# Kernel optimization log

Hardware: AMD Instinct MI355X
Metric: run time of the kernel (lower is better)

## Reference

```python
import jax, jax.numpy as jnp
import numpy as np

RENORM_PERIOD = 256
MAX_NORM = 100.0


def setup_inputs() -> dict:
    key = jax.random.key(0)
    ks = jax.random.split(key, 9)
    B, S, G, D, N = 4, 2048, 8, 128, 64
    return {
        "x_r": jax.random.normal(ks[0], (B, S, G, D), jnp.float32),
        "x_i": jax.random.normal(ks[1], (B, S, G, D), jnp.float32),
        "log_A_mag": jax.random.uniform(ks[2], (G, N), jnp.float32) * 0.5 + 0.5,
        "A_phase": jax.random.normal(ks[3], (G, N), jnp.float32) * 0.1,
        "Bw_r": jax.random.normal(ks[4], (N, D), jnp.float32) / np.sqrt(D),
        "Bw_i": jax.random.normal(ks[5], (N, D), jnp.float32) / np.sqrt(D),
        "Cw_r": jax.random.normal(ks[6], (D, N), jnp.float32) / np.sqrt(N),
        "Cw_i": jax.random.normal(ks[7], (D, N), jnp.float32) / np.sqrt(N),
        "dt_w": jax.random.normal(ks[8], (2, 2 * D), jnp.float32) * 0.02,
        "dt_b": jnp.zeros((2,), jnp.float32),
    }


def reference(x_r, x_i, log_A_mag, A_phase, Bw_r, Bw_i, Cw_r, Cw_i, dt_w, dt_b):
    B, S, G, D = x_r.shape
    N = Bw_r.shape[0]
    # dt: input-dependent step magnitude / phase scale, clamped
    x_cat = jnp.concatenate([x_r, x_i], axis=-1)            # [B,S,G,2D]
    dt = jnp.clip(jnp.exp(jnp.einsum('bsgd,od->bsgo', x_cat, dt_w) + dt_b), 1e-4, 2.0)
    dt_mag = dt[..., 0:1]                                    # [B,S,G,1]
    dt_phase = dt[..., 1:2]
    # A_bar in polar form, |A| = exp(-softplus(log_A_mag)*dt_mag) < 1
    neg_log_A = -jax.nn.softplus(log_A_mag)[None, None]      # [1,1,G,N]
    A_mag = jnp.exp(dt_mag * neg_log_A)                      # [B,S,G,N]
    A_ang = dt_phase * A_phase[None, None]
    A_r = A_mag * jnp.cos(A_ang)
    A_i = A_mag * jnp.sin(A_ang)
    # Bx = (B_proj @ x) * dt_mag, complex linear
    Bx_r = (jnp.einsum('bsgd,nd->bsgn', x_r, Bw_r) - jnp.einsum('bsgd,nd->bsgn', x_i, Bw_i)) * dt_mag
    Bx_i = (jnp.einsum('bsgd,nd->bsgn', x_r, Bw_i) + jnp.einsum('bsgd,nd->bsgn', x_i, Bw_r)) * dt_mag

    def step(carry, inp):
        h_r, h_i = carry
        ar, ai, br, bi, t = inp
        nh_r = ar * h_r - ai * h_i + br
        nh_i = ar * h_i + ai * h_r + bi
        renorm = ((t + 1) % RENORM_PERIOD) == 0
        norm = jnp.sqrt(nh_r * nh_r + nh_i * nh_i + 1e-8)
        scale = jnp.minimum(norm, MAX_NORM) / norm
        nh_r = jnp.where(renorm, nh_r * scale, nh_r)
        nh_i = jnp.where(renorm, nh_i * scale, nh_i)
        return (nh_r, nh_i), (nh_r, nh_i)

    h0 = (jnp.zeros((B, G, N), jnp.float32), jnp.zeros((B, G, N), jnp.float32))
    xs = (jnp.moveaxis(A_r, 1, 0), jnp.moveaxis(A_i, 1, 0),
          jnp.moveaxis(Bx_r, 1, 0), jnp.moveaxis(Bx_i, 1, 0),
          jnp.arange(S))
    _, (all_h_r, all_h_i) = jax.lax.scan(step, h0, xs)       # [S,B,G,N]
    all_h_r = jnp.moveaxis(all_h_r, 0, 1)                    # [B,S,G,N]
    all_h_i = jnp.moveaxis(all_h_i, 0, 1)
    # y = C_proj(h), complex linear N -> D
    y_r = jnp.einsum('bsgn,dn->bsgd', all_h_r, Cw_r) - jnp.einsum('bsgn,dn->bsgd', all_h_i, Cw_i)
    y_i = jnp.einsum('bsgn,dn->bsgd', all_h_r, Cw_i) + jnp.einsum('bsgn,dn->bsgd', all_h_i, Cw_r)
    return jnp.stack([y_r, y_i], axis=0)                     # [2,B,S,G,D]
```

## Files before the change

### kernel.cpp

```cpp
#include <hip/hip_runtime.h>
#include <math.h>

#define B_ 4
#define S_ 2048
#define G_ 8
#define D_ 128
#define N_ 64
#define ROWS (B_*S_*G_)
#define CH 64
#define CLEN 32
#define NCHAIN (B_*G_*N_)
#define YOFF (ROWS*D_)

typedef short bf16x8 __attribute__((ext_vector_type(8)));
typedef float f32x4  __attribute__((ext_vector_type(4)));
#define MFMA16(a,b,c) __builtin_amdgcn_mfma_f32_16x16x32_bf16(a,b,c,0,0,0)

__device__ __forceinline__ unsigned short bf16_rtne(float f) {
    unsigned u = __float_as_uint(f);
    unsigned r = (u + 0x7FFFu + ((u >> 16) & 1u)) >> 16;
    return (unsigned short)r;
}
__device__ __forceinline__ void split_bf16(float f, unsigned short &hi, unsigned short &lo) {
    hi = bf16_rtne(f);
    float hif = __uint_as_float(((unsigned)hi) << 16);
    lo = bf16_rtne(f - hif);
}
__device__ __forceinline__ unsigned pk_bf16(float a, float b) {
    unsigned r;
    asm("v_cvt_pk_bf16_f32 %0, %1, %2" : "=v"(r) : "v"(a), "v"(b));
    return r;
}
__device__ __forceinline__ void split4_pk(float4 v, uint2 &hi2, uint2 &lo2) {
    unsigned p0 = pk_bf16(v.x, v.y);
    unsigned p1 = pk_bf16(v.z, v.w);
    float r0 = v.x - __uint_as_float(p0 << 16);
    float r1 = v.y - __uint_as_float(p0 & 0xFFFF0000u);
    float r2 = v.z - __uint_as_float(p1 << 16);
    float r3 = v.w - __uint_as_float(p1 & 0xFFFF0000u);
    hi2 = make_uint2(p0, p1);
    lo2 = make_uint2(pk_bf16(r0, r1), pk_bf16(r2, r3));
}
__device__ __forceinline__ float dot4(float4 a, float4 b) {
    return fmaf(a.x,b.x, fmaf(a.y,b.y, fmaf(a.z,b.z, a.w*b.w)));
}

__global__ __launch_bounds__(256) void k_prep(
    const float* __restrict__ bwr, const float* __restrict__ bwi,
    const float* __restrict__ cwr, const float* __restrict__ cwi,
    unsigned short* __restrict__ wbhi, unsigned short* __restrict__ wblo,
    unsigned short* __restrict__ wchi)
{
    int tid = blockIdx.x * 256 + threadIdx.x;
    if (tid < 4096) {
        int f = tid;
        int lane = f & 63, ks = (f >> 6) & 7, nt = (f >> 9) & 1, w = f >> 10;
        int l15 = lane & 15, quad = lane >> 4;
        int n = w * 32 + nt * 16 + l15;
        int k0 = ks * 32 + quad * 8;
        const float* src; float sgn = 1.f;
        if (n < 64) {
            if (k0 < 128) src = bwr + n * 128 + k0;
            else        { src = bwi + n * 128 + (k0 - 128); sgn = -1.f; }
        } else {
            if (k0 < 128) src = bwi + (n - 64) * 128 + k0;
            else          src = bwr + (n - 64) * 128 + (k0 - 128);
        }
        float4 v0 = *(const float4*)src;
        float4 v1 = *(const float4*)(src + 4);
        float vv[8] = {v0.x,v0.y,v0.z,v0.w,v1.x,v1.y,v1.z,v1.w};
        unsigned short h[8], l[8];
        #pragma unroll
        for (int j = 0; j < 8; j++) split_bf16(vv[j] * sgn, h[j], l[j]);
        #pragma unroll
        for (int j = 0; j < 8; j++) { wbhi[f*8+j] = h[j]; wblo[f*8+j] = l[j]; }
    } else {
        int f = tid - 4096;
        int lane = f & 63, ks = (f >> 6) & 3, nt = (f >> 8) & 3, w = f >> 10;
        int l15 = lane & 15, quad = lane >> 4;
        int n = w * 64 + nt * 16 + l15;
        int d = (n < 128) ? n : (n - 128);
        int k0 = ks * 32 + quad * 8;
        unsigned short h[8];
        #pragma unroll
        for (int j = 0; j < 8; j++) {
            int k = k0 + j, col = k >> 1;
            float val;
            if (n < 128) val = (k & 1) ? -cwi[d * 64 + col] : cwr[d * 64 + col];
            else         val = (k & 1) ?  cwr[d * 64 + col] : cwi[d * 64 + col];
            unsigned short hh, hl; split_bf16(val, hh, hl);
            h[j] = hh;
        }
        #pragma unroll
        for (int j = 0; j < 8; j++) wchi[f*8+j] = h[j];
    }
}

#define LDK1 280
__global__ __launch_bounds__(256, 4) void k_g1(
    const float* __restrict__ xr, const float* __restrict__ xi,
    const float* __restrict__ dtw, const float* __restrict__ dtb,
    const float* __restrict__ logAm, const float* __restrict__ Aph,
    const unsigned short* __restrict__ wbhi, const unsigned short* __restrict__ wblo,
    float* __restrict__ bxr, float* __restrict__ bxi,
    float* __restrict__ dt_mag, float* __restrict__ dt_ph,
    float4* __restrict__ trans)
{
    __shared__ __align__(16) unsigned short Ahi[32 * LDK1];
    __shared__ __align__(16) unsigned short Alo[32 * LDK1];
    __shared__ float dms[32], dps[32];
    __shared__ float4 comb[64];
    float* bxs = (float*)Ahi;
    const int t = threadIdx.x;
    const int lane = t & 63, w = t >> 6;
    const int l15 = lane & 15, quad = lane >> 4;
    const int bg = blockIdx.x >> 6, c = blockIdx.x & 63;
    const int g = bg & 7, b = bg >> 3;
    const int crow = (bg * CH + c) * CLEN;

    const int kq = t & 31, k4 = kq * 4;
    float4 w0r = *(const float4*)(dtw + k4);
    float4 w0i = *(const float4*)(dtw + 128 + k4);
    float4 w1r = *(const float4*)(dtw + 256 + k4);
    float4 w1i = *(const float4*)(dtw + 384 + k4);
    float b0 = dtb[0], b1 = dtb[1];
    float nla = -logf(1.0f + __expf(logAm[g * N_ + lane]));
    float aph = Aph[g * N_ + lane];

    const int s0 = c * CLEN;
    const float* xrb = xr + ((size_t)(b * S_ + s0) * G_ + g) * 128;
    const float* xib = xi + ((size_t)(b * S_ + s0) * G_ + g) * 128;

    float pm[4], pp[4];
    #pragma unroll
    for (int i = 0; i < 4; i++) {
        int f = t + 256 * i;
        int m = f >> 5, kk = f & 31;
        float4 a  = ((const float4*)(xrb + m * 1024))[kk];
        float4 bb = ((const float4*)(xib + m * 1024))[kk];
        uint2 h2, l2;
        split4_pk(a, h2, l2);
        *(uint2*)&Ahi[m * LDK1 + kk * 4] = h2;
        *(uint2*)&Alo[m * LDK1 + kk * 4] = l2;
        split4_pk(bb, h2, l2);
        *(uint2*)&Ahi[m * LDK1 + 128 + kk * 4] = h2;
        *(uint2*)&Alo[m * LDK1 + 128 + kk * 4] = l2;
        pm[i] = dot4(a, w0r) + dot4(bb, w0i);
        pp[i] = dot4(a, w1r) + dot4(bb, w1i);
    }
    #pragma unroll
    for (int i = 0; i < 4; i++) {
        float vm = pm[i], vp = pp[i];
        #pragma unroll
        for (int msk = 16; msk >= 1; msk >>= 1) {
            vm += __shfl_xor(vm, msk);
            vp += __shfl_xor(vp, msk);
        }
        if ((t & 31) == 0) {
            int m = (t >> 5) + 8 * i;
            float dm = fminf(fmaxf(__expf(vm + b0), 1e-4f), 2.0f);
            float dp = fminf(fmaxf(__expf(vp + b1), 1e-4f), 2.0f);
            dms[m] = dm; dps[m] = dp;
            dt_mag[crow + m] = dm; dt_ph[crow + m] = dp;
        }
    }
    __syncthreads();

    f32x4 acc[2][2];
    #pragma unroll
    for (int a = 0; a < 2; a++)
        #pragma unroll
        for (int bq = 0; bq < 2; bq++)
            acc[a][bq] = (f32x4){0.f, 0.f, 0.f, 0.f};
    #pragma unroll
    for (int ks = 0; ks < 8; ks++) {
        bf16x8 wh0 = ((const bf16x8*)wbhi)[((w * 2 + 0) * 8 + ks) * 64 + lane];
        bf16x8 wl0 = ((const bf16x8*)wblo)[((w * 2 + 0) * 8 + ks) * 64 + lane];
        bf16x8 wh1 = ((const bf16x8*)wbhi)[((w * 2 + 1) * 8 + ks) * 64 + lane];
        bf16x8 wl1 = ((const bf16x8*)wblo)[((w * 2 + 1) * 8 + ks) * 64 + lane];
        #pragma unroll
        for (int ms = 0; ms < 2; ms++) {
            int arow = (ms * 16 + l15) * LDK1 + quad * 8;
            bf16x8 ah = *(const bf16x8*)&Ahi[arow + ks * 32];
            bf16x8 al = *(const bf16x8*)&Alo[arow + ks * 32];
            acc[ms][0] = MFMA16(al, wh0, acc[ms][0]);
            acc[ms][0] = MFMA16(ah, wl0, acc[ms][0]);
            acc[ms][0] = MFMA16(ah, wh0, acc[ms][0]);
            acc[ms][1] = MFMA16(al, wh1, acc[ms][1]);
            acc[ms][1] = MFMA16(ah, wl1, acc[ms][1]);
            acc[ms][1] = MFMA16(ah, wh1, acc[ms][1]);
        }
    }
    __syncthreads();

    #pragma unroll
    for (int ms = 0; ms < 2; ms++)
        #pragma unroll
        for (int nt = 0; nt < 2; nt++) {
            int n = w * 32 + nt * 16 + l15;
            float* dstg = (n < 64) ? bxr : bxi;
            int nn = n & 63;
            #pragma unroll
            for (int r = 0; r < 4; r++) {
                int m = ms * 16 + quad * 4 + r;
                float v = acc[ms][nt][r] * dms[m];
                dstg[(crow + m) * 64 + nn] = v;
                bxs[m * 132 + n] = v;
            }
        }
    __syncthreads();

    float Ar = 1.f, Ai = 0.f, Br = 0.f, Bi = 0.f;
    if (w < 2) {
        int base = w * 16;
        #pragma unroll
        for (int tt = 0; tt < 16; tt++) {
            int m = base + tt;
            float dm = dms[m], dp = dps[m];
            float am  = __expf(dm * nla);
            float ang = dp * aph;
            float cr = am * __cosf(ang), ci = am * __sinf(ang);
            float vr = bxs[m * 132 + lane], vi = bxs[m * 132 + 64 + lane];
            float nAr = cr * Ar - ci * Ai;
            float nAi = cr * Ai + ci * Ar;
            float nBr = cr * Br - ci * Bi + vr;
            float nBi = cr * Bi + ci * Br + vi;
            Ar = nAr; Ai = nAi; Br = nBr; Bi = nBi;
        }
        if (w == 0) comb[lane] = make_float4(Ar, Ai, Br, Bi);
    }
    __syncthreads();
    if (w == 1) {
        float4 c0 = comb[lane];
        float fAr = Ar * c0.x - Ai * c0.y;
        float fAi = Ar * c0.y + Ai * c0.x;
        float fBr = Ar * c0.z - Ai * c0.w + Br;
        float fBi = Ar * c0.w + Ai * c0.z + Bi;
        trans[(bg * CH + c) * 64 + lane] = make_float4(fAr, fAi, fBr, fBi);
    }
}

__global__ __launch_bounds__(256) void k_scanB2(const float4* __restrict__ trans,
    float2* __restrict__ hstart)
{
    int w = threadIdx.x >> 6, lane = threadIdx.x & 63;
    int W = blockIdx.x * 4 + w;
    int bg = W >> 3;
    int n  = ((W & 7) << 3) + (lane & 7);
    int j  = lane >> 3;
    float pAr[8], pAi[8], pBr[8], pBi[8];
    float Ar = 1.f, Ai = 0.f, Br = 0.f, Bi = 0.f;
    const float4* tp = trans + (bg * CH + j * 8) * 64 + n;
    #pragma unroll
    for (int k = 0; k < 8; k++) {
        pAr[k] = Ar; pAi[k] = Ai; pBr[k] = Br; pBi[k] = Bi;
        float4 T = tp[k * 64];
        float nAr = T.x * Ar - T.y * Ai;
        float nAi = T.x * Ai + T.y * Ar;
        float nBr = T.x * Br - T.y * Bi + T.z;
        float nBi = T.x * Bi + T.y * Br + T.w;
        Ar = nAr; Ai = nAi; Br = nBr; Bi = nBi;
    }
    float hr = 0.f, hi = 0.f, mhr = 0.f, mhi = 0.f;
    #pragma unroll
    for (int j2 = 0; j2 < 8; j2++) {
        if (j2 == j) { mhr = hr; mhi = hi; }
        int src = j2 * 8 + (lane & 7);
        float sAr = __shfl(Ar, src), sAi = __shfl(Ai, src);
        float sBr = __shfl(Br, src), sBi = __shfl(Bi, src);
        float nr = sAr * hr - sAi * hi + sBr;
        float ni = sAr * hi + sAi * hr + sBi;
        float nrm = sqrtf(nr * nr + ni * ni + 1e-8f);
        float sc = fminf(nrm, 100.f) / nrm;
        hr = nr * sc; hi = ni * sc;
    }
    float2* hp = hstart + (bg * CH + j * 8) * 64 + n;
    #pragma unroll
    for (int k = 0; k < 8; k++) {
        float hsr = pAr[k] * mhr - pAi[k] * mhi + pBr[k];
        float hsi = pAr[k] * mhi + pAi[k] * mhr + pBi[k];
        hp[k * 64] = make_float2(hsr, hsi);
    }
}

#define LDK2 152
__global__ __launch_bounds__(256, 6) void k_sg2(
    const float* __restrict__ bxr, const float* __restrict__ bxi,
    const float* __restrict__ dt_mag, const float* __restrict__ dt_ph,
    const float* __restrict__ logAm, const float* __restrict__ Aph,
    const float2* __restrict__ hstart,
    const unsigned short* __restrict__ wchi,
    float* __restrict__ out)
{
    __shared__ __align__(16) unsigned short Ahi[32 * LDK2];
    __shared__ __align__(16) unsigned short Alo[32 * LDK2];
    const int t = threadIdx.x;
    const int lane = t & 63, w = t >> 6;
    const int l15 = lane & 15, quad = lane >> 4;
    const int bg = blockIdx.x >> 6, c = blockIdx.x & 63;
    const int g = bg & 7, b = bg >> 3;

    if (w == 0) {
        const int n = lane;
        float nla = -logf(1.0f + __expf(logAm[g * N_ + n]));
        float aph = Aph[g * N_ + n];
        float2 h0 = hstart[(bg * CH + c) * 64 + n];
        float hr = h0.x, hi = h0.y;
        const bool rn = ((c & 7) == 7);
        const int base = (bg * CH + c) * CLEN;
        #pragma unroll 8
        for (int tt = 0; tt < CLEN; tt++) {
            float dm = dt_mag[base + tt], dp = dt_ph[base + tt];
            float am  = __expf(dm * nla);
            float ang = dp * aph;
            float cr = am * __cosf(ang), ci = am * __sinf(ang);
            float vr = bxr[(base + tt) * 64 + n];
            float vi = bxi[(base + tt) * 64 + n];
            float nr = cr * hr - ci * hi + vr;
            float ni = cr * hi + ci * hr + vi;
            if (rn && tt == CLEN - 1) {
                float nrm = sqrtf(nr * nr + ni * ni + 1e-8f);
                float scale = fminf(nrm, 100.0f) / nrm;
                nr *= scale; ni *= scale;
            }
            hr = nr; hi = ni;
            unsigned hp = pk_bf16(hr, hi);
            float rr = hr - __uint_as_float(hp << 16);
            float ri = hi - __uint_as_float(hp & 0xFFFF0000u);
            unsigned lp = pk_bf16(rr, ri);
            *(unsigned*)&Ahi[tt * LDK2 + 2 * n] = hp;
            *(unsigned*)&Alo[tt * LDK2 + 2 * n] = lp;
        }
    }
    __syncthreads();

    f32x4 acc[2][4];
    #pragma unroll
    for (int a = 0; a < 2; a++)
        #pragma unroll
        for (int bq = 0; bq < 4; bq++)
            acc[a][bq] = (f32x4){0.f, 0.f, 0.f, 0.f};
    #pragma unroll
    for (int ks = 0; ks < 4; ks++) {
        bf16x8 wc0 = ((const bf16x8*)wchi)[((w * 4 + 0) * 4 + ks) * 64 + lane];
        bf16x8 wc1 = ((const bf16x8*)wchi)[((w * 4 + 1) * 4 + ks) * 64 + lane];
        bf16x8 wc2 = ((const bf16x8*)wchi)[((w * 4 + 2) * 4 + ks) * 64 + lane];
        bf16x8 wc3 = ((const bf16x8*)wchi)[((w * 4 + 3) * 4 + ks) * 64 + lane];
        #pragma unroll
        for (int ms = 0; ms < 2; ms++) {
            int arow = (ms * 16 + l15) * LDK2 + quad * 8;
            bf16x8 ah = *(const bf16x8*)&Ahi[arow + ks * 32];
            bf16x8 al = *(const bf16x8*)&Alo[arow + ks * 32];
            acc[ms][0] = MFMA16(al, wc0, acc[ms][0]);
            acc[ms][0] = MFMA16(ah, wc0, acc[ms][0]);
            acc[ms][1] = MFMA16(al, wc1, acc[ms][1]);
            acc[ms][1] = MFMA16(ah, wc1, acc[ms][1]);
            acc[ms][2] = MFMA16(al, wc2, acc[ms][2]);
            acc[ms][2] = MFMA16(ah, wc2, acc[ms][2]);
            acc[ms][3] = MFMA16(al, wc3, acc[ms][3]);
            acc[ms][3] = MFMA16(ah, wc3, acc[ms][3]);
        }
    }
    #pragma unroll
    for (int ms = 0; ms < 2; ms++)
        #pragma unroll
        for (int nt = 0; nt < 4; nt++) {
            int nn = w * 64 + nt * 16 + l15;
            float* dst = (nn < 128) ? (out + nn) : (out + YOFF + (nn - 128));
            #pragma unroll
            for (int r = 0; r < 4; r++) {
                int tt2 = ms * 16 + quad * 4 + r;
                int srow = (b * S_ + c * CLEN + tt2) * G_ + g;
                dst[srow * 128] = acc[ms][nt][r];
            }
        }
}

extern "C" void kernel_launch(void* const* d_in, const int* in_sizes, int n_in,
                              void* d_out, int out_size, void* d_ws, size_t ws_size,
                              hipStream_t stream) {
    (void)in_sizes; (void)n_in; (void)out_size; (void)ws_size;
    const float* xr    = (const float*)d_in[0];
    const float* xi    = (const float*)d_in[1];
    const float* logAm = (const float*)d_in[2];
    const float* Aph   = (const float*)d_in[3];
    const float* bwr   = (const float*)d_in[4];
    const float* bwi   = (const float*)d_in[5];
    const float* cwr   = (const float*)d_in[6];
    const float* cwi   = (const float*)d_in[7];
    const float* dtw   = (const float*)d_in[8];
    const float* dtb   = (const float*)d_in[9];
    float* out = (float*)d_out;
    float* ws  = (float*)d_ws;

    float*  dt_mag = ws;
    float*  dt_ph  = ws + 65536;
    float*  bxr    = ws + 131072;
    float*  bxi    = bxr + 4194304;
    float4* trans  = (float4*)(ws + 8519680);
    float2* hstart = (float2*)(ws + 9043968);
    unsigned short* wbhi = (unsigned short*)(ws + 9306112);
    unsigned short* wblo = wbhi + 32768;
    unsigned short* wchi = wblo + 32768;

    hipLaunchKernelGGL(k_prep,   dim3(32), dim3(256), 0, stream,
                       bwr, bwi, cwr, cwi, wbhi, wblo, wchi);
    hipLaunchKernelGGL(k_g1,     dim3((B_ * G_) * 64), dim3(256), 0, stream,
                       xr, xi, dtw, dtb, logAm, Aph, wbhi, wblo,
                       bxr, bxi, dt_mag, dt_ph, trans);
    hipLaunchKernelGGL(k_scanB2, dim3(64), dim3(256), 0, stream,
                       trans, hstart);
    hipLaunchKernelGGL(k_sg2,    dim3((B_ * G_) * 64), dim3(256), 0, stream,
                       bxr, bxi, dt_mag, dt_ph, logAm, Aph, hstart, wchi, out);
}
```

Before: 165.2 us.

## Fuse projection, chunked scan and output GEMM into one cooperative kernel

Replaces the three-kernel pipeline (B-projection plus chunk transitions, cross-chunk scan, rescan plus C-projection) with one cooperative kernel that keeps Bx and dt values in shared memory and uses a grid-wide sync between the chunk-summary phase and the per-chunk rescan. The intent is to stop writing and rereading the large Bx, dt intermediates through global memory and to cut launch overhead. Each block now redundantly walks the prefix of chunk transitions itself, with periodic renormalisation, instead of relying on a separate scan kernel. The risks are the cost of the grid sync, a longer serial prefix walk for later chunks, and a dependence on all 1024 blocks being co-resident; the old path is kept as a fallback.

```diff
diff --git a/kernel.cpp b/kernel.cpp
--- a/kernel.cpp
+++ b/kernel.cpp
@@ -1,5 +1,8 @@
 #include <hip/hip_runtime.h>
+#include <hip/hip_cooperative_groups.h>
 #include <math.h>
+
+namespace cg = cooperative_groups;
 
 #define B_ 4
 #define S_ 2048
@@ -9,7 +12,6 @@
 #define ROWS (B_*S_*G_)
 #define CH 64
 #define CLEN 32
-#define NCHAIN (B_*G_*N_)
 #define YOFF (ROWS*D_)
 
 typedef short bf16x8 __attribute__((ext_vector_type(8)));
@@ -93,6 +95,249 @@
         }
         #pragma unroll
         for (int j = 0; j < 8; j++) wchi[f*8+j] = h[j];
+    }
+}
+
+#define UROW 156
+__global__ __launch_bounds__(256, 4) void k_fused(
+    const float* __restrict__ xr, const float* __restrict__ xi,
+    const float* __restrict__ dtw, const float* __restrict__ dtb,
+    const float* __restrict__ logAm, const float* __restrict__ Aph,
+    const unsigned short* __restrict__ wbhi, const unsigned short* __restrict__ wblo,
+    const unsigned short* __restrict__ wchi,
+    float4* __restrict__ trans,
+    float* __restrict__ out)
+{
+    __shared__ __align__(16) unsigned U[64 * UROW];
+    __shared__ float dms[64], dps[64];
+    float* Uf = (float*)U;
+    unsigned short* SH = (unsigned short*)U;
+
+    const int t = threadIdx.x;
+    const int lane = t & 63, w = t >> 6;
+    const int l15 = lane & 15, quad = lane >> 4;
+    const int bg = blockIdx.x >> 5, cp = blockIdx.x & 31;
+    const int g = bg & 7, b = bg >> 3;
+    const int cA = cp * 2;
+
+    const float b0 = dtb[0], b1 = dtb[1];
+    const float nla = -logf(1.0f + __expf(logAm[g * N_ + lane]));
+    const float aph = Aph[g * N_ + lane];
+
+    f32x4 acc[2][2][2];
+    #pragma unroll
+    for (int q = 0; q < 2; q++)
+        #pragma unroll
+        for (int a = 0; a < 2; a++)
+            #pragma unroll
+            for (int bq = 0; bq < 2; bq++)
+                acc[q][a][bq] = (f32x4){0.f, 0.f, 0.f, 0.f};
+
+    #pragma unroll 1
+    for (int q = 0; q < 2; q++) {
+        const int c = cA + q;
+        const float* xrb = xr + ((size_t)(b * S_ + c * CLEN) * G_ + g) * 128;
+        const float* xib = xi + ((size_t)(b * S_ + c * CLEN) * G_ + g) * 128;
+        const int q16 = t & 15;
+        #pragma unroll
+        for (int i = 0; i < 2; i++) {
+            const int m = (t >> 4) + 16 * i;
+            const float* src = (q16 < 8) ? (xrb + m * 1024 + q16 * 16)
+                                         : (xib + m * 1024 + (q16 - 8) * 16);
+            float4 v0 = ((const float4*)src)[0];
+            float4 v1 = ((const float4*)src)[1];
+            float4 v2 = ((const float4*)src)[2];
+            float4 v3 = ((const float4*)src)[3];
+            const float* w0p = dtw + q16 * 16;
+            const float* w1p = dtw + 256 + q16 * 16;
+            float pm = dot4(v0, ((const float4*)w0p)[0]) + dot4(v1, ((const float4*)w0p)[1])
+                     + dot4(v2, ((const float4*)w0p)[2]) + dot4(v3, ((const float4*)w0p)[3]);
+            float pp = dot4(v0, ((const float4*)w1p)[0]) + dot4(v1, ((const float4*)w1p)[1])
+                     + dot4(v2, ((const float4*)w1p)[2]) + dot4(v3, ((const float4*)w1p)[3]);
+            uint2 h2, l2;
+            split4_pk(v0, h2, l2);
+            *(uint2*)&SH[m * 264 + q16 * 16 + 0]        = h2;
+            *(uint2*)&SH[8448 + m * 264 + q16 * 16 + 0] = l2;
+            split4_pk(v1, h2, l2);
+            *(uint2*)&SH[m * 264 + q16 * 16 + 4]        = h2;
+            *(uint2*)&SH[8448 + m * 264 + q16 * 16 + 4] = l2;
+            split4_pk(v2, h2, l2);
+            *(uint2*)&SH[m * 264 + q16 * 16 + 8]        = h2;
+            *(uint2*)&SH[8448 + m * 264 + q16 * 16 + 8] = l2;
+            split4_pk(v3, h2, l2);
+            *(uint2*)&SH[m * 264 + q16 * 16 + 12]        = h2;
+            *(uint2*)&SH[8448 + m * 264 + q16 * 16 + 12] = l2;
+            #pragma unroll
+            for (int msk = 8; msk >= 1; msk >>= 1) {
+                pm += __shfl_xor(pm, msk);
+                pp += __shfl_xor(pp, msk);
+            }
+            if (q16 == 0) {
+                float dm = fminf(fmaxf(__expf(pm + b0), 1e-4f), 2.0f);
+                float dp = fminf(fmaxf(__expf(pp + b1), 1e-4f), 2.0f);
+                dms[q * 32 + m] = dm; dps[q * 32 + m] = dp;
+            }
+        }
+        __syncthreads();
+        #pragma unroll
+        for (int ks = 0; ks < 8; ks++) {
+            bf16x8 wh0 = ((const bf16x8*)wbhi)[((w * 2 + 0) * 8 + ks) * 64 + lane];
+            bf16x8 wl0 = ((const bf16x8*)wblo)[((w * 2 + 0) * 8 + ks) * 64 + lane];
+            bf16x8 wh1 = ((const bf16x8*)wbhi)[((w * 2 + 1) * 8 + ks) * 64 + lane];
+            bf16x8 wl1 = ((const bf16x8*)wblo)[((w * 2 + 1) * 8 + ks) * 64 + lane];
+            #pragma unroll
+            for (int ms = 0; ms < 2; ms++) {
+                const int ro = (ms * 16 + l15) * 264 + ks * 32 + quad * 8;
+                bf16x8 ah = *(const bf16x8*)&SH[ro];
+                bf16x8 al = *(const bf16x8*)&SH[8448 + ro];
+                acc[q][ms][0] = MFMA16(al, wh0, acc[q][ms][0]);
+                acc[q][ms][0] = MFMA16(ah, wl0, acc[q][ms][0]);
+                acc[q][ms][0] = MFMA16(ah, wh0, acc[q][ms][0]);
+                acc[q][ms][1] = MFMA16(al, wh1, acc[q][ms][1]);
+                acc[q][ms][1] = MFMA16(ah, wl1, acc[q][ms][1]);
+                acc[q][ms][1] = MFMA16(ah, wh1, acc[q][ms][1]);
+            }
+        }
+        __syncthreads();
+    }
+
+    #pragma unroll
+    for (int q = 0; q < 2; q++)
+        #pragma unroll
+        for (int ms = 0; ms < 2; ms++)
+            #pragma unroll
+            for (int nt = 0; nt < 2; nt++) {
+                const int n = w * 32 + nt * 16 + l15;
+                #pragma unroll
+                for (int r = 0; r < 4; r++) {
+                    const int m32 = ms * 16 + quad * 4 + r;
+                    Uf[(q * 32 + m32) * UROW + 28 + n] =
+                        acc[q][ms][nt][r] * dms[q * 32 + m32];
+                }
+            }
+    __syncthreads();
+
+    {
+        const int q = w >> 1, half = w & 1;
+        float Ar = 1.f, Ai = 0.f, Br = 0.f, Bi = 0.f;
+        #pragma unroll
+        for (int tt = 0; tt < 16; tt++) {
+            const int m = q * 32 + half * 16 + tt;
+            float dm = dms[m], dp = dps[m];
+            float am  = __expf(dm * nla);
+            float ang = dp * aph;
+            float cr = am * __cosf(ang), ci = am * __sinf(ang);
+            float vr = Uf[m * UROW + 28 + lane];
+            float vi = Uf[m * UROW + 92 + lane];
+            float nAr = cr * Ar - ci * Ai;
+            float nAi = cr * Ai + ci * Ar;
+            float nBr = cr * Br - ci * Bi + vr;
+            float nBi = cr * Bi + ci * Br + vi;
+            Ar = nAr; Ai = nAi; Br = nBr; Bi = nBi;
+        }
+        if (half == 0)
+            *(float4*)&Uf[lane * UROW + 4 * q] = make_float4(Ar, Ai, Br, Bi);
+        __syncthreads();
+        if (half == 1) {
+            float4 c0 = *(float4*)&Uf[lane * UROW + 4 * q];
+            float fAr = Ar * c0.x - Ai * c0.y;
+            float fAi = Ar * c0.y + Ai * c0.x;
+            float fBr = Ar * c0.z - Ai * c0.w + Br;
+            float fBi = Ar * c0.w + Ai * c0.z + Bi;
+            trans[(bg * CH + cA + q) * 64 + lane] = make_float4(fAr, fAi, fBr, fBi);
+        }
+    }
+
+    cg::this_grid().sync();
+
+    if (w == 0) {
+        float shr = 0.f, shi = 0.f;
+        const float4* tp = trans + (size_t)(bg * CH) * 64 + lane;
+        int cc = 0;
+        while (cc + 8 <= cA) {
+            float4 T[8];
+            #pragma unroll
+            for (int k = 0; k < 8; k++) T[k] = tp[(cc + k) * 64];
+            #pragma unroll
+            for (int k = 0; k < 8; k++) {
+                float nr = T[k].x * shr - T[k].y * shi + T[k].z;
+                float ni = T[k].x * shi + T[k].y * shr + T[k].w;
+                shr = nr; shi = ni;
+            }
+            float nrm = sqrtf(shr * shr + shi * shi + 1e-8f);
+            float sc = fminf(nrm, 100.f) / nrm;
+            shr *= sc; shi *= sc;
+            cc += 8;
+        }
+        for (; cc < cA; cc++) {
+            float4 T = tp[cc * 64];
+            float nr = T.x * shr - T.y * shi + T.z;
+            float ni = T.x * shi + T.y * shr + T.w;
+            shr = nr; shi = ni;
+        }
+        const bool rnB = (((cA + 1) & 7) == 7);
+        #pragma unroll 8
+        for (int tt = 0; tt < 64; tt++) {
+            float dm = dms[tt], dp = dps[tt];
+            float am  = __expf(dm * nla);
+            float ang = dp * aph;
+            float cr = am * __cosf(ang), ci = am * __sinf(ang);
+            float vr = Uf[tt * UROW + 28 + lane];
+            float vi = Uf[tt * UROW + 92 + lane];
+            float nr = cr * shr - ci * shi + vr;
+            float ni = cr * shi + ci * shr + vi;
+            if (rnB && tt == 63) {
+                float nrm = sqrtf(nr * nr + ni * ni + 1e-8f);
+                float scale = fminf(nrm, 100.0f) / nrm;
+                nr *= scale; ni *= scale;
+            }
+            shr = nr; shi = ni;
+            unsigned hp = pk_bf16(shr, shi);
+            float rr = shr - __uint_as_float(hp << 16);
+            float ri = shi - __uint_as_float(hp & 0xFFFF0000u);
+            unsigned lp = pk_bf16(rr, ri);
+            *(unsigned*)&SH[tt * 312 + 2 * lane]       = hp;
+            *(unsigned*)&SH[tt * 312 + 152 + 2 * lane] = lp;
+        }
+    }
+    __syncthreads();
+
+    #pragma unroll 1
+    for (int p = 0; p < 2; p++) {
+        f32x4 a2[4][2];
+        #pragma unroll
+        for (int a = 0; a < 4; a++)
+            #pragma unroll
+            for (int bq = 0; bq < 2; bq++)
+                a2[a][bq] = (f32x4){0.f, 0.f, 0.f, 0.f};
+        #pragma unroll
+        for (int ks = 0; ks < 4; ks++) {
+            bf16x8 wc0 = ((const bf16x8*)wchi)[((w * 4 + p * 2 + 0) * 4 + ks) * 64 + lane];
+            bf16x8 wc1 = ((const bf16x8*)wchi)[((w * 4 + p * 2 + 1) * 4 + ks) * 64 + lane];
+            #pragma unroll
+            for (int ms = 0; ms < 4; ms++) {
+                const int ro = (ms * 16 + l15) * 312 + ks * 32 + quad * 8;
+                bf16x8 ah = *(const bf16x8*)&SH[ro];
+                bf16x8 al = *(const bf16x8*)&SH[ro + 152];
+                a2[ms][0] = MFMA16(al, wc0, a2[ms][0]);
+                a2[ms][0] = MFMA16(ah, wc0, a2[ms][0]);
+                a2[ms][1] = MFMA16(al, wc1, a2[ms][1]);
+                a2[ms][1] = MFMA16(ah, wc1, a2[ms][1]);
+            }
+        }
+        #pragma unroll
+        for (int ms = 0; ms < 4; ms++)
+            #pragma unroll
+            for (int ntl = 0; ntl < 2; ntl++) {
+                const int nn = (w * 4 + p * 2 + ntl) * 16 + l15;
+                float* dst = (nn < 128) ? (out + nn) : (out + YOFF + (nn - 128));
+                #pragma unroll
+                for (int r = 0; r < 4; r++) {
+                    const int ml = ms * 16 + quad * 4 + r;
+                    const int srow = (b * S_ + cA * CLEN + ml) * G_ + g;
+                    dst[(size_t)srow * 128] = a2[ms][ntl][r];
+                }
+            }
     }
 }
 
@@ -403,13 +648,42 @@
     unsigned short* wblo = wbhi + 32768;
     unsigned short* wchi = wblo + 32768;
 
-    hipLaunchKernelGGL(k_prep,   dim3(32), dim3(256), 0, stream,
+    hipLaunchKernelGGL(k_prep, dim3(32), dim3(256), 0, stream,
                        bwr, bwi, cwr, cwi, wbhi, wblo, wchi);
-    hipLaunchKernelGGL(k_g1,     dim3((B_ * G_) * 64), dim3(256), 0, stream,
-                       xr, xi, dtw, dtb, logAm, Aph, wbhi, wblo,
-                       bxr, bxi, dt_mag, dt_ph, trans);
-    hipLaunchKernelGGL(k_scanB2, dim3(64), dim3(256), 0, stream,
-                       trans, hstart);
-    hipLaunchKernelGGL(k_sg2,    dim3((B_ * G_) * 64), dim3(256), 0, stream,
-                       bxr, bxi, dt_mag, dt_ph, logAm, Aph, hstart, wchi, out);
-}
+
+    bool fused_ok = false;
+    int dev = 0;
+    if (hipGetDevice(&dev) == hipSuccess) {
+        int coop = 0, ncu = 0, nb = 0;
+        hipDeviceGetAttribute(&coop, hipDeviceAttributeCooperativeLaunch, dev);
+        hipDeviceGetAttribute(&ncu, hipDeviceAttributeMultiprocessorCount, dev);
+        hipError_t oe = hipOccupancyMaxActiveBlocksPerMultiprocessor(
+            &nb, reinterpret_cast<const void*>(k_fused), 256, 0);
+        if (coop && oe == hipSuccess && (long)nb * (long)ncu >= 1024) {
+            const unsigned short* wbhi_c = wbhi;
+            const unsigned short* wblo_c = wblo;
+            const unsigned short* wchi_c = wchi;
+            void* args[] = {
+                (void*)&xr, (void*)&xi, (void*)&dtw, (void*)&dtb,
+                (void*)&logAm, (void*)&Aph,
+                (void*)&wbhi_c, (void*)&wblo_c, (void*)&wchi_c,
+                (void*)&trans, (void*)&out
+            };
+            hipError_t e = hipLaunchCooperativeKernel(
+                reinterpret_cast<void*>(k_fused), dim3(1024), dim3(256),
+                args, 0, stream);
+            if (e == hipSuccess) fused_ok = true;
+            else (void)hipGetLastError();
+        }
+    }
+
+    if (!fused_ok) {
+        hipLaunchKernelGGL(k_g1, dim3((B_ * G_) * 64), dim3(256), 0, stream,
+                           xr, xi, dtw, dtb, logAm, Aph, wbhi, wblo,
+                           bxr, bxi, dt_mag, dt_ph, trans);
+        hipLaunchKernelGGL(k_scanB2, dim3(64), dim3(256), 0, stream,
+                           trans, hstart);
+        hipLaunchKernelGGL(k_sg2, dim3((B_ * G_) * 64), dim3(256), 0, stream,
+                           bxr, bxi, dt_mag, dt_ph, logAm, Aph, hstart, wchi, out);
+    }
+}
```

New measurement: 160.3 us. -3.0%, faster.

## Single-wave output kernel, four-wave chunk scan, and prefetched weights in projection

Applied to the files above, without the earlier changes.

The final kernel now runs with one wave per block: the same wave computes the chunk's hidden states and then loops over four column panels of the C projection. This removes the block barrier and the three idle waves that previously waited on the scan. In the first kernel, the B-projection weight fragments are software-prefetched one k-step ahead, and the intra-chunk scan is split across all four waves (8 steps each) and combined through shared memory. Output stores become nontemporal. The risks are less parallelism per block in the output kernel and more register pressure from the prefetch.

```diff
diff --git a/kernel.cpp b/kernel.cpp
--- a/kernel.cpp
+++ b/kernel.cpp
@@ -9,7 +9,6 @@
 #define ROWS (B_*S_*G_)
 #define CH 64
 #define CLEN 32
-#define NCHAIN (B_*G_*N_)
 #define YOFF (ROWS*D_)
 
 typedef short bf16x8 __attribute__((ext_vector_type(8)));
@@ -109,7 +108,7 @@
     __shared__ __align__(16) unsigned short Ahi[32 * LDK1];
     __shared__ __align__(16) unsigned short Alo[32 * LDK1];
     __shared__ float dms[32], dps[32];
-    __shared__ float4 comb[64];
+    __shared__ float4 comb[192];
     float* bxs = (float*)Ahi;
     const int t = threadIdx.x;
     const int lane = t & 63, w = t >> 6;
@@ -126,6 +125,11 @@
     float b0 = dtb[0], b1 = dtb[1];
     float nla = -logf(1.0f + __expf(logAm[g * N_ + lane]));
     float aph = Aph[g * N_ + lane];
+
+    const bf16x8* WHp = (const bf16x8*)wbhi + (w * 2) * 512 + lane;
+    const bf16x8* WLp = (const bf16x8*)wblo + (w * 2) * 512 + lane;
+    bf16x8 wh0 = WHp[0],   wl0 = WLp[0];
+    bf16x8 wh1 = WHp[512], wl1 = WLp[512];
 
     const int s0 = c * CLEN;
     const float* xrb = xr + ((size_t)(b * S_ + s0) * G_ + g) * 128;
@@ -174,10 +178,11 @@
             acc[a][bq] = (f32x4){0.f, 0.f, 0.f, 0.f};
     #pragma unroll
     for (int ks = 0; ks < 8; ks++) {
-        bf16x8 wh0 = ((const bf16x8*)wbhi)[((w * 2 + 0) * 8 + ks) * 64 + lane];
-        bf16x8 wl0 = ((const bf16x8*)wblo)[((w * 2 + 0) * 8 + ks) * 64 + lane];
-        bf16x8 wh1 = ((const bf16x8*)wbhi)[((w * 2 + 1) * 8 + ks) * 64 + lane];
-        bf16x8 wl1 = ((const bf16x8*)wblo)[((w * 2 + 1) * 8 + ks) * 64 + lane];
+        bf16x8 nh0, nl0, nh1, nl1;
+        if (ks < 7) {
+            nh0 = WHp[(ks + 1) * 64];        nl0 = WLp[(ks + 1) * 64];
+            nh1 = WHp[512 + (ks + 1) * 64];  nl1 = WLp[512 + (ks + 1) * 64];
+        }
         #pragma unroll
         for (int ms = 0; ms < 2; ms++) {
             int arow = (ms * 16 + l15) * LDK1 + quad * 8;
@@ -190,6 +195,7 @@
             acc[ms][1] = MFMA16(ah, wl1, acc[ms][1]);
             acc[ms][1] = MFMA16(ah, wh1, acc[ms][1]);
         }
+        if (ks < 7) { wh0 = nh0; wl0 = nl0; wh1 = nh1; wl1 = nl1; }
     }
     __syncthreads();
 
@@ -210,12 +216,12 @@
         }
     __syncthreads();
 
-    float Ar = 1.f, Ai = 0.f, Br = 0.f, Bi = 0.f;
-    if (w < 2) {
-        int base = w * 16;
-        #pragma unroll
-        for (int tt = 0; tt < 16; tt++) {
-            int m = base + tt;
+    {
+        float Ar = 1.f, Ai = 0.f, Br = 0.f, Bi = 0.f;
+        const int base = w * 8;
+        #pragma unroll
+        for (int tt = 0; tt < 8; tt++) {
+            const int m = base + tt;
             float dm = dms[m], dp = dps[m];
             float am  = __expf(dm * nla);
             float ang = dp * aph;
@@ -227,16 +233,26 @@
             float nBi = cr * Bi + ci * Br + vi;
             Ar = nAr; Ai = nAi; Br = nBr; Bi = nBi;
         }
-        if (w == 0) comb[lane] = make_float4(Ar, Ai, Br, Bi);
-    }
-    __syncthreads();
-    if (w == 1) {
-        float4 c0 = comb[lane];
-        float fAr = Ar * c0.x - Ai * c0.y;
-        float fAi = Ar * c0.y + Ai * c0.x;
-        float fBr = Ar * c0.z - Ai * c0.w + Br;
-        float fBi = Ar * c0.w + Ai * c0.z + Bi;
-        trans[(bg * CH + c) * 64 + lane] = make_float4(fAr, fAi, fBr, fBi);
+        if (w < 3) comb[w * 64 + lane] = make_float4(Ar, Ai, Br, Bi);
+        __syncthreads();
+        if (w == 3) {
+            float4 c0 = comb[lane];
+            float cAr = c0.x, cAi = c0.y, cBr = c0.z, cBi = c0.w;
+            #pragma unroll
+            for (int s = 1; s < 3; s++) {
+                float4 ps = comb[s * 64 + lane];
+                float nAr = ps.x * cAr - ps.y * cAi;
+                float nAi = ps.x * cAi + ps.y * cAr;
+                float nBr = ps.x * cBr - ps.y * cBi + ps.z;
+                float nBi = ps.x * cBi + ps.y * cBr + ps.w;
+                cAr = nAr; cAi = nAi; cBr = nBr; cBi = nBi;
+            }
+            float fAr = Ar * cAr - Ai * cAi;
+            float fAi = Ar * cAi + Ai * cAr;
+            float fBr = Ar * cBr - Ai * cBi + Br;
+            float fBi = Ar * cBi + Ai * cBr + Bi;
+            trans[(bg * CH + c) * 64 + lane] = make_float4(fAr, fAi, fBr, fBi);
+        }
     }
 }
 
@@ -283,8 +299,9 @@
     }
 }
 
-#define LDK2 152
-__global__ __launch_bounds__(256, 6) void k_sg2(
+#define LDW 132
+#define HALFW 4224
+__global__ __launch_bounds__(64, 4) void k_sg3(
     const float* __restrict__ bxr, const float* __restrict__ bxi,
     const float* __restrict__ dt_mag, const float* __restrict__ dt_ph,
     const float* __restrict__ logAm, const float* __restrict__ Aph,
@@ -292,15 +309,13 @@
     const unsigned short* __restrict__ wchi,
     float* __restrict__ out)
 {
-    __shared__ __align__(16) unsigned short Ahi[32 * LDK2];
-    __shared__ __align__(16) unsigned short Alo[32 * LDK2];
-    const int t = threadIdx.x;
-    const int lane = t & 63, w = t >> 6;
+    __shared__ __align__(16) unsigned short A[2 * HALFW];
+    const int lane = threadIdx.x;
     const int l15 = lane & 15, quad = lane >> 4;
     const int bg = blockIdx.x >> 6, c = blockIdx.x & 63;
     const int g = bg & 7, b = bg >> 3;
 
-    if (w == 0) {
+    {
         const int n = lane;
         float nla = -logf(1.0f + __expf(logAm[g * N_ + n]));
         float aph = Aph[g * N_ + n];
@@ -328,52 +343,54 @@
             float rr = hr - __uint_as_float(hp << 16);
             float ri = hi - __uint_as_float(hp & 0xFFFF0000u);
             unsigned lp = pk_bf16(rr, ri);
-            *(unsigned*)&Ahi[tt * LDK2 + 2 * n] = hp;
-            *(unsigned*)&Alo[tt * LDK2 + 2 * n] = lp;
-        }
-    }
-    __syncthreads();
-
-    f32x4 acc[2][4];
-    #pragma unroll
-    for (int a = 0; a < 2; a++)
-        #pragma unroll
-        for (int bq = 0; bq < 4; bq++)
-            acc[a][bq] = (f32x4){0.f, 0.f, 0.f, 0.f};
-    #pragma unroll
-    for (int ks = 0; ks < 4; ks++) {
-        bf16x8 wc0 = ((const bf16x8*)wchi)[((w * 4 + 0) * 4 + ks) * 64 + lane];
-        bf16x8 wc1 = ((const bf16x8*)wchi)[((w * 4 + 1) * 4 + ks) * 64 + lane];
-        bf16x8 wc2 = ((const bf16x8*)wchi)[((w * 4 + 2) * 4 + ks) * 64 + lane];
-        bf16x8 wc3 = ((const bf16x8*)wchi)[((w * 4 + 3) * 4 + ks) * 64 + lane];
-        #pragma unroll
-        for (int ms = 0; ms < 2; ms++) {
-            int arow = (ms * 16 + l15) * LDK2 + quad * 8;
-            bf16x8 ah = *(const bf16x8*)&Ahi[arow + ks * 32];
-            bf16x8 al = *(const bf16x8*)&Alo[arow + ks * 32];
-            acc[ms][0] = MFMA16(al, wc0, acc[ms][0]);
-            acc[ms][0] = MFMA16(ah, wc0, acc[ms][0]);
-            acc[ms][1] = MFMA16(al, wc1, acc[ms][1]);
-            acc[ms][1] = MFMA16(ah, wc1, acc[ms][1]);
-            acc[ms][2] = MFMA16(al, wc2, acc[ms][2]);
-            acc[ms][2] = MFMA16(ah, wc2, acc[ms][2]);
-            acc[ms][3] = MFMA16(al, wc3, acc[ms][3]);
-            acc[ms][3] = MFMA16(ah, wc3, acc[ms][3]);
-        }
-    }
-    #pragma unroll
-    for (int ms = 0; ms < 2; ms++)
-        #pragma unroll
-        for (int nt = 0; nt < 4; nt++) {
-            int nn = w * 64 + nt * 16 + l15;
-            float* dst = (nn < 128) ? (out + nn) : (out + YOFF + (nn - 128));
+            *(unsigned*)&A[tt * LDW + 2 * n]         = hp;
+            *(unsigned*)&A[HALFW + tt * LDW + 2 * n] = lp;
+        }
+    }
+
+    #pragma unroll 1
+    for (int P = 0; P < 4; P++) {
+        f32x4 acc[2][4];
+        #pragma unroll
+        for (int a = 0; a < 2; a++)
             #pragma unroll
-            for (int r = 0; r < 4; r++) {
-                int tt2 = ms * 16 + quad * 4 + r;
-                int srow = (b * S_ + c * CLEN + tt2) * G_ + g;
-                dst[srow * 128] = acc[ms][nt][r];
+            for (int j = 0; j < 4; j++)
+                acc[a][j] = (f32x4){0.f, 0.f, 0.f, 0.f};
+        #pragma unroll
+        for (int ks = 0; ks < 4; ks++) {
+            bf16x8 wc0 = ((const bf16x8*)wchi)[(P * 1024) + 0 * 256 + ks * 64 + lane];
+            bf16x8 wc1 = ((const bf16x8*)wchi)[(P * 1024) + 1 * 256 + ks * 64 + lane];
+            bf16x8 wc2 = ((const bf16x8*)wchi)[(P * 1024) + 2 * 256 + ks * 64 + lane];
+            bf16x8 wc3 = ((const bf16x8*)wchi)[(P * 1024) + 3 * 256 + ks * 64 + lane];
+            #pragma unroll
+            for (int ms = 0; ms < 2; ms++) {
+                int arow = (ms * 16 + l15) * LDW + ks * 32 + quad * 8;
+                bf16x8 ah = *(const bf16x8*)&A[arow];
+                bf16x8 al = *(const bf16x8*)&A[HALFW + arow];
+                acc[ms][0] = MFMA16(al, wc0, acc[ms][0]);
+                acc[ms][0] = MFMA16(ah, wc0, acc[ms][0]);
+                acc[ms][1] = MFMA16(al, wc1, acc[ms][1]);
+                acc[ms][1] = MFMA16(ah, wc1, acc[ms][1]);
+                acc[ms][2] = MFMA16(al, wc2, acc[ms][2]);
+                acc[ms][2] = MFMA16(ah, wc2, acc[ms][2]);
+                acc[ms][3] = MFMA16(al, wc3, acc[ms][3]);
+                acc[ms][3] = MFMA16(ah, wc3, acc[ms][3]);
             }
         }
+        #pragma unroll
+        for (int ms = 0; ms < 2; ms++)
+            #pragma unroll
+            for (int j = 0; j < 4; j++) {
+                int nn = P * 64 + j * 16 + l15;
+                float* dst = (nn < 128) ? (out + nn) : (out + YOFF + (nn - 128));
+                #pragma unroll
+                for (int r = 0; r < 4; r++) {
+                    int tt2 = ms * 16 + quad * 4 + r;
+                    int srow = (b * S_ + c * CLEN + tt2) * G_ + g;
+                    __builtin_nontemporal_store(acc[ms][j][r], &dst[(size_t)srow * 128]);
+                }
+            }
+    }
 }
 
 extern "C" void kernel_launch(void* const* d_in, const int* in_sizes, int n_in,
@@ -410,6 +427,6 @@
                        bxr, bxi, dt_mag, dt_ph, trans);
     hipLaunchKernelGGL(k_scanB2, dim3(64), dim3(256), 0, stream,
                        trans, hstart);
-    hipLaunchKernelGGL(k_sg2,    dim3((B_ * G_) * 64), dim3(256), 0, stream,
+    hipLaunchKernelGGL(k_sg3,    dim3((B_ * G_) * 64), dim3(64), 0, stream,
                        bxr, bxi, dt_mag, dt_ph, logAm, Aph, hstart, wchi, out);
 }
```

New measurement: 168.1 us. No clear change (+1.8%).

## Use single bf16 for B projection, prefetch weights, split chunk scan across four waves

Applied to the files above, without the earlier changes.

The B-projection GEMM in k_g1 drops the hi/lo bf16 split compensation and uses one bf16 MFMA per tile instead of three. This removes the Alo shared buffer and the lo-weight loads, and the smaller shared-memory footprint allows occupancy of 8 blocks per CU. Weight fragments are now prefetched one k-step ahead. The intra-chunk transition scan is spread over all four waves, each handling 8 steps, and then combined. The trade-off is lower precision in Bx, which may break tolerance over a 2048-step recurrence.

```diff
diff --git a/kernel.cpp b/kernel.cpp
--- a/kernel.cpp
+++ b/kernel.cpp
@@ -9,7 +9,6 @@
 #define ROWS (B_*S_*G_)
 #define CH 64
 #define CLEN 32
-#define NCHAIN (B_*G_*N_)
 #define YOFF (ROWS*D_)
 
 typedef short bf16x8 __attribute__((ext_vector_type(8)));
@@ -30,16 +29,6 @@
     unsigned r;
     asm("v_cvt_pk_bf16_f32 %0, %1, %2" : "=v"(r) : "v"(a), "v"(b));
     return r;
-}
-__device__ __forceinline__ void split4_pk(float4 v, uint2 &hi2, uint2 &lo2) {
-    unsigned p0 = pk_bf16(v.x, v.y);
-    unsigned p1 = pk_bf16(v.z, v.w);
-    float r0 = v.x - __uint_as_float(p0 << 16);
-    float r1 = v.y - __uint_as_float(p0 & 0xFFFF0000u);
-    float r2 = v.z - __uint_as_float(p1 << 16);
-    float r3 = v.w - __uint_as_float(p1 & 0xFFFF0000u);
-    hi2 = make_uint2(p0, p1);
-    lo2 = make_uint2(pk_bf16(r0, r1), pk_bf16(r2, r3));
 }
 __device__ __forceinline__ float dot4(float4 a, float4 b) {
     return fmaf(a.x,b.x, fmaf(a.y,b.y, fmaf(a.z,b.z, a.w*b.w)));
@@ -96,20 +85,19 @@
     }
 }
 
-#define LDK1 280
-__global__ __launch_bounds__(256, 4) void k_g1(
+#define LDK1 264
+__global__ __launch_bounds__(256, 8) void k_g1(
     const float* __restrict__ xr, const float* __restrict__ xi,
     const float* __restrict__ dtw, const float* __restrict__ dtb,
     const float* __restrict__ logAm, const float* __restrict__ Aph,
-    const unsigned short* __restrict__ wbhi, const unsigned short* __restrict__ wblo,
+    const unsigned short* __restrict__ wbhi,
     float* __restrict__ bxr, float* __restrict__ bxi,
     float* __restrict__ dt_mag, float* __restrict__ dt_ph,
     float4* __restrict__ trans)
 {
     __shared__ __align__(16) unsigned short Ahi[32 * LDK1];
-    __shared__ __align__(16) unsigned short Alo[32 * LDK1];
+    __shared__ float4 comb[192];
     __shared__ float dms[32], dps[32];
-    __shared__ float4 comb[64];
     float* bxs = (float*)Ahi;
     const int t = threadIdx.x;
     const int lane = t & 63, w = t >> 6;
@@ -127,6 +115,10 @@
     float nla = -logf(1.0f + __expf(logAm[g * N_ + lane]));
     float aph = Aph[g * N_ + lane];
 
+    const bf16x8* WHp = (const bf16x8*)wbhi + (w * 2) * 512 + lane;
+    bf16x8 wh0 = WHp[0];
+    bf16x8 wh1 = WHp[512];
+
     const int s0 = c * CLEN;
     const float* xrb = xr + ((size_t)(b * S_ + s0) * G_ + g) * 128;
     const float* xib = xi + ((size_t)(b * S_ + s0) * G_ + g) * 128;
@@ -138,13 +130,11 @@
         int m = f >> 5, kk = f & 31;
         float4 a  = ((const float4*)(xrb + m * 1024))[kk];
         float4 bb = ((const float4*)(xib + m * 1024))[kk];
-        uint2 h2, l2;
-        split4_pk(a, h2, l2);
+        uint2 h2;
+        h2 = make_uint2(pk_bf16(a.x, a.y), pk_bf16(a.z, a.w));
         *(uint2*)&Ahi[m * LDK1 + kk * 4] = h2;
-        *(uint2*)&Alo[m * LDK1 + kk * 4] = l2;
-        split4_pk(bb, h2, l2);
+        h2 = make_uint2(pk_bf16(bb.x, bb.y), pk_bf16(bb.z, bb.w));
         *(uint2*)&Ahi[m * LDK1 + 128 + kk * 4] = h2;
-        *(uint2*)&Alo[m * LDK1 + 128 + kk * 4] = l2;
         pm[i] = dot4(a, w0r) + dot4(bb, w0i);
         pp[i] = dot4(a, w1r) + dot4(bb, w1i);
     }
@@ -174,22 +164,19 @@
             acc[a][bq] = (f32x4){0.f, 0.f, 0.f, 0.f};
     #pragma unroll
     for (int ks = 0; ks < 8; ks++) {
-        bf16x8 wh0 = ((const bf16x8*)wbhi)[((w * 2 + 0) * 8 + ks) * 64 + lane];
-        bf16x8 wl0 = ((const bf16x8*)wblo)[((w * 2 + 0) * 8 + ks) * 64 + lane];
-        bf16x8 wh1 = ((const bf16x8*)wbhi)[((w * 2 + 1) * 8 + ks) * 64 + lane];
-        bf16x8 wl1 = ((const bf16x8*)wblo)[((w * 2 + 1) * 8 + ks) * 64 + lane];
+        bf16x8 nh0, nh1;
+        if (ks < 7) {
+            nh0 = WHp[(ks + 1) * 64];
+            nh1 = WHp[512 + (ks + 1) * 64];
+        }
         #pragma unroll
         for (int ms = 0; ms < 2; ms++) {
             int arow = (ms * 16 + l15) * LDK1 + quad * 8;
             bf16x8 ah = *(const bf16x8*)&Ahi[arow + ks * 32];
-            bf16x8 al = *(const bf16x8*)&Alo[arow + ks * 32];
-            acc[ms][0] = MFMA16(al, wh0, acc[ms][0]);
-            acc[ms][0] = MFMA16(ah, wl0, acc[ms][0]);
             acc[ms][0] = MFMA16(ah, wh0, acc[ms][0]);
-            acc[ms][1] = MFMA16(al, wh1, acc[ms][1]);
-            acc[ms][1] = MFMA16(ah, wl1, acc[ms][1]);
             acc[ms][1] = MFMA16(ah, wh1, acc[ms][1]);
         }
+        if (ks < 7) { wh0 = nh0; wh1 = nh1; }
     }
     __syncthreads();
 
@@ -210,12 +197,12 @@
         }
     __syncthreads();
 
-    float Ar = 1.f, Ai = 0.f, Br = 0.f, Bi = 0.f;
-    if (w < 2) {
-        int base = w * 16;
-        #pragma unroll
-        for (int tt = 0; tt < 16; tt++) {
-            int m = base + tt;
+    {
+        float Ar = 1.f, Ai = 0.f, Br = 0.f, Bi = 0.f;
+        const int base = w * 8;
+        #pragma unroll
+        for (int tt = 0; tt < 8; tt++) {
+            const int m = base + tt;
             float dm = dms[m], dp = dps[m];
             float am  = __expf(dm * nla);
             float ang = dp * aph;
@@ -227,16 +214,26 @@
             float nBi = cr * Bi + ci * Br + vi;
             Ar = nAr; Ai = nAi; Br = nBr; Bi = nBi;
         }
-        if (w == 0) comb[lane] = make_float4(Ar, Ai, Br, Bi);
-    }
-    __syncthreads();
-    if (w == 1) {
-        float4 c0 = comb[lane];
-        float fAr = Ar * c0.x - Ai * c0.y;
-        float fAi = Ar * c0.y + Ai * c0.x;
-        float fBr = Ar * c0.z - Ai * c0.w + Br;
-        float fBi = Ar * c0.w + Ai * c0.z + Bi;
-        trans[(bg * CH + c) * 64 + lane] = make_float4(fAr, fAi, fBr, fBi);
+        if (w < 3) comb[w * 64 + lane] = make_float4(Ar, Ai, Br, Bi);
+        __syncthreads();
+        if (w == 3) {
+            float4 c0 = comb[lane];
+            float cAr = c0.x, cAi = c0.y, cBr = c0.z, cBi = c0.w;
+            #pragma unroll
+            for (int s = 1; s < 3; s++) {
+                float4 ps = comb[s * 64 + lane];
+                float nAr = ps.x * cAr - ps.y * cAi;
+                float nAi = ps.x * cAi + ps.y * cAr;
+                float nBr = ps.x * cBr - ps.y * cBi + ps.z;
+                float nBi = ps.x * cBi + ps.y * cBr + ps.w;
+                cAr = nAr; cAi = nAi; cBr = nBr; cBi = nBi;
+            }
+            float fAr = Ar * cAr - Ai * cAi;
+            float fAi = Ar * cAi + Ai * cAr;
+            float fBr = Ar * cBr - Ai * cBi + Br;
+            float fBi = Ar * cBi + Ai * cBr + Bi;
+            trans[(bg * CH + c) * 64 + lane] = make_float4(fAr, fAi, fBr, fBi);
+        }
     }
 }
 
@@ -406,7 +403,7 @@
     hipLaunchKernelGGL(k_prep,   dim3(32), dim3(256), 0, stream,
                        bwr, bwi, cwr, cwi, wbhi, wblo, wchi);
     hipLaunchKernelGGL(k_g1,     dim3((B_ * G_) * 64), dim3(256), 0, stream,
-                       xr, xi, dtw, dtb, logAm, Aph, wbhi, wblo,
+                       xr, xi, dtw, dtb, logAm, Aph, wbhi,
                        bxr, bxi, dt_mag, dt_ph, trans);
     hipLaunchKernelGGL(k_scanB2, dim3(64), dim3(256), 0, stream,
                        trans, hstart);
```

Result: no change. 168.4 us (+2.0%).
